# Kernel tuning notes

Measured on AMD Instinct MI355X. Metric: run time of the kernel, lower is better.

The kernel has to match this reference:

```python
import jax, jax.numpy as jnp
import numpy as np

D_MODEL = 2048
N_HEADS = 16
HEAD_DIM = D_MODEL // N_HEADS
B, T = 2, 2048


def setup_inputs() -> dict:
    key = jax.random.key(0)
    ks = jax.random.split(key, 7)
    s = 0.02
    return {
        "x": jax.random.normal(ks[0], (B, T, D_MODEL), dtype=jnp.float32),
        "w_qkv": jax.random.normal(ks[1], (D_MODEL, 3 * D_MODEL), dtype=jnp.float32) * s,
        "w_proj": jax.random.normal(ks[2], (D_MODEL, D_MODEL), dtype=jnp.float32) * s,
        "w_ff1": jax.random.normal(ks[3], (D_MODEL, 4 * D_MODEL), dtype=jnp.float32) * s,
        "b_ff1": jnp.zeros((4 * D_MODEL,), dtype=jnp.float32),
        "w_ff2": jax.random.normal(ks[4], (4 * D_MODEL, D_MODEL), dtype=jnp.float32) * s,
        "b_ff2": jnp.zeros((D_MODEL,), dtype=jnp.float32),
    }


def reference(x, w_qkv, w_proj, w_ff1, b_ff1, w_ff2, b_ff2):
    Bs, Ts, C = x.shape
    H, hd = N_HEADS, HEAD_DIM
    # fused qkv projection
    qkv = jnp.einsum("btc,cd->btd", x, w_qkv)
    q, k, v = jnp.split(qkv, 3, axis=-1)
    # (B, T, C) -> (B, H, T, hd)
    q = q.reshape(Bs, Ts, H, hd).transpose(0, 2, 1, 3)
    k = k.reshape(Bs, Ts, H, hd).transpose(0, 2, 1, 3)
    v = v.reshape(Bs, Ts, H, hd).transpose(0, 2, 1, 3)
    # paged KV write + gather round-trip (empty cache, n_kv_head == n_heads)
    # is the identity on k, v; attention is causal SDPA over the full cache.
    scale = 1.0 / jnp.sqrt(jnp.asarray(hd, dtype=x.dtype))
    scores = jnp.einsum("bhqd,bhkd->bhqk", q, k) * scale
    causal = jnp.tril(jnp.ones((Ts, Ts), dtype=bool))
    scores = jnp.where(causal, scores, jnp.finfo(scores.dtype).min)
    attn = jax.nn.softmax(scores, axis=-1)
    out = jnp.einsum("bhqk,bhkd->bhqd", attn, v)  # (B, H, T, hd)
    out = out.transpose(0, 2, 1, 3).reshape(Bs, Ts, C)
    attn_out = jnp.einsum("btc,cd->btd", out, w_proj)
    # feed-forward with exact GELU (torch nn.GELU default)
    h = jax.nn.gelu(jnp.einsum("btc,cf->btf", x, w_ff1) + b_ff1, approximate=False)
    ff_out = jnp.einsum("btf,fc->btc", h, w_ff2) + b_ff2
    return x + attn_out + ff_out
```

## Files before the change

kernel.cpp:

```cpp
#include <hip/hip_runtime.h>
#include <hip/hip_bf16.h>
#include <cmath>

typedef __bf16 bf16x8 __attribute__((ext_vector_type(8)));
typedef float f32x4 __attribute__((ext_vector_type(4)));
typedef unsigned short u16;
typedef unsigned int u32;

#define DEV __device__ __forceinline__

static constexpr int BB = 2;
static constexpr int T = 2048;
static constexpr int DM = 2048;
static constexpr int NH = 16;
static constexpr int HD = 128;
static constexpr int FF = 8192;
static constexpr int M = BB * T;
static constexpr int NQKV = 3 * DM;

DEV u16 f2b(float f) {
  u32 u = __builtin_bit_cast(u32, f);
  u = (u + 0x7FFFu + ((u >> 16) & 1u)) >> 16;
  return (u16)u;
}
DEV float b2f(u16 h) {
  u32 u = ((u32)h) << 16;
  return __builtin_bit_cast(float, u);
}

DEV void gload16(const u16* g, const u16* l) {
  __builtin_amdgcn_global_load_lds(
      (const __attribute__((address_space(1))) void*)(uintptr_t)g,
      (__attribute__((address_space(3))) void*)(unsigned)(uintptr_t)l,
      16, 0, 0);
}


__global__ void cvt_f32_to_bf16(const float* __restrict__ in, u16* __restrict__ out, int n4) {
  int i = blockIdx.x * blockDim.x + threadIdx.x;
  if (i >= n4) return;
  float4 v = reinterpret_cast<const float4*>(in)[i];
  ushort4 o;
  o.x = f2b(v.x); o.y = f2b(v.y); o.z = f2b(v.z); o.w = f2b(v.w);
  reinterpret_cast<ushort4*>(out)[i] = o;
}

__global__ void transpose_cvt(const float* __restrict__ W, u16* __restrict__ Wt, int K, int N) {
  __shared__ float tile[32][33];
  int nb = blockIdx.x * 32, kb = blockIdx.y * 32;
  int tx = threadIdx.x & 31, ty = threadIdx.x >> 5;
#pragma unroll
  for (int r = 0; r < 32; r += 8)
    tile[ty + r][tx] = W[(size_t)(kb + ty + r) * N + nb + tx];
  __syncthreads();
#pragma unroll
  for (int r = 0; r < 32; r += 8)
    Wt[(size_t)(nb + ty + r) * K + kb + tx] = f2b(tile[tx][ty + r]);
}

template <int EPI>
__global__ __launch_bounds__(512, 2) void gemm8(
    const u16* __restrict__ A, const u16* __restrict__ Bt, int Ndim, int K, int gx,
    u16* __restrict__ out_bf, const float* __restrict__ bias) {
  __shared__ __align__(16) u16 lds[2 * 32768];
  const int t = threadIdx.x;
  const int nwg = gridDim.x, cpx = nwg >> 3;
  const int wg = (blockIdx.x & 7) * cpx + (blockIdx.x >> 3);
  const int m0 = (wg / gx) * 256, n0 = (wg % gx) * 256;
  const int wave = t >> 6, lane = t & 63;
  const int wm = wave >> 2, wn = wave & 3;
  const int lr = lane & 15, lk = lane >> 4;

  const int srow = t >> 3;
  const int sc8 = ((t & 7) ^ (srow & 7)) * 8;
  const u16* gA = &A[(size_t)(m0 + srow) * K + sc8];
  const u16* gB = &Bt[(size_t)(n0 + srow) * K + sc8];
  const int wls = wave * 512;

  u16* buf0 = lds;
  u16* buf1 = lds + 32768;

#define STAGE_A(buf, h, kt)                                                      \
  {                                                                              \
    gload16(gA + (size_t)((h) * 128) * K + (kt) * 64, (buf) + (h) * 8192 + wls); \
    gload16(gA + (size_t)((h) * 128 + 64) * K + (kt) * 64,                       \
            (buf) + (h) * 8192 + 4096 + wls);                                    \
  }
#define STAGE_B(buf, h, kt)                                                      \
  {                                                                              \
    gload16(gB + (size_t)((h) * 128) * K + (kt) * 64,                            \
            (buf) + 16384 + (h) * 8192 + wls);                                   \
    gload16(gB + (size_t)((h) * 128 + 64) * K + (kt) * 64,                       \
            (buf) + 16384 + (h) * 8192 + 4096 + wls);                            \
  }
#define PH_PRE                          \
  __builtin_amdgcn_sched_barrier(0);    \
  __builtin_amdgcn_s_barrier();         \
  __builtin_amdgcn_sched_barrier(0);    \
  __builtin_amdgcn_s_setprio(1);
#define PH_POST                         \
  __builtin_amdgcn_s_setprio(0);        \
  __builtin_amdgcn_sched_barrier(0);    \
  __builtin_amdgcn_s_barrier();         \
  __builtin_amdgcn_sched_barrier(0);

  const int NT = K >> 6;

  STAGE_A(buf0, 0, 0); STAGE_A(buf0, 1, 0);
  STAGE_B(buf0, 0, 0); STAGE_B(buf0, 1, 0);
  STAGE_A(buf1, 0, 1); STAGE_B(buf1, 0, 1);
  __builtin_amdgcn_sched_barrier(0);
  asm volatile("s_waitcnt vmcnt(4)" ::: "memory");
  __builtin_amdgcn_s_barrier();
  __builtin_amdgcn_sched_barrier(0);

  f32x4 acc[8][4] = {};
  const int aBase = (wm * 128 + lr) * 64;
  const int bBase = 16384 + (wn * 64 + lr) * 64;
  const int c0 = (lk ^ (lr & 7)) * 8;
  const int c1 = ((4 + lk) ^ (lr & 7)) * 8;

  u16* cur = buf0;
  u16* alt = buf1;
  bf16x8 af[4][2], bq0[2][2], bq1[2][2];

  for (int kt = 0; kt < NT; ++kt) {
#pragma unroll
    for (int i = 0; i < 4; ++i) {
      af[i][0] = *(const bf16x8*)&cur[aBase + i * 1024 + c0];
      af[i][1] = *(const bf16x8*)&cur[aBase + i * 1024 + c1];
    }
#pragma unroll
    for (int j = 0; j < 2; ++j) {
      bq0[j][0] = *(const bf16x8*)&cur[bBase + j * 1024 + c0];
      bq0[j][1] = *(const bf16x8*)&cur[bBase + j * 1024 + c1];
    }
    if (kt + 1 < NT) STAGE_A(alt, 1, kt + 1);
    PH_PRE;
#pragma unroll
    for (int i = 0; i < 4; ++i)
#pragma unroll
      for (int j = 0; j < 2; ++j)
#pragma unroll
        for (int kk = 0; kk < 2; ++kk)
          acc[i][j] = __builtin_amdgcn_mfma_f32_16x16x32_bf16(af[i][kk], bq0[j][kk], acc[i][j], 0, 0, 0);
    PH_POST;
#pragma unroll
    for (int j = 0; j < 2; ++j) {
      bq1[j][0] = *(const bf16x8*)&cur[bBase + (2 + j) * 1024 + c0];
      bq1[j][1] = *(const bf16x8*)&cur[bBase + (2 + j) * 1024 + c1];
    }
    if (kt + 1 < NT) STAGE_B(alt, 1, kt + 1);
    PH_PRE;
#pragma unroll
    for (int i = 0; i < 4; ++i)
#pragma unroll
      for (int j = 0; j < 2; ++j)
#pragma unroll
        for (int kk = 0; kk < 2; ++kk)
          acc[i][2 + j] = __builtin_amdgcn_mfma_f32_16x16x32_bf16(af[i][kk], bq1[j][kk], acc[i][2 + j], 0, 0, 0);
    PH_POST;
#pragma unroll
    for (int i = 0; i < 4; ++i) {
      af[i][0] = *(const bf16x8*)&cur[aBase + (4 + i) * 1024 + c0];
      af[i][1] = *(const bf16x8*)&cur[aBase + (4 + i) * 1024 + c1];
    }
    if (kt + 2 < NT) STAGE_A(cur, 0, kt + 2);
    PH_PRE;
#pragma unroll
    for (int i = 0; i < 4; ++i)
#pragma unroll
      for (int j = 0; j < 2; ++j)
#pragma unroll
        for (int kk = 0; kk < 2; ++kk)
          acc[4 + i][2 + j] = __builtin_amdgcn_mfma_f32_16x16x32_bf16(af[i][kk], bq1[j][kk], acc[4 + i][2 + j], 0, 0, 0);
    PH_POST;
    if (kt + 2 < NT) STAGE_B(cur, 0, kt + 2);
    PH_PRE;
#pragma unroll
    for (int i = 0; i < 4; ++i)
#pragma unroll
      for (int j = 0; j < 2; ++j)
#pragma unroll
        for (int kk = 0; kk < 2; ++kk)
          acc[4 + i][j] = __builtin_amdgcn_mfma_f32_16x16x32_bf16(af[i][kk], bq0[j][kk], acc[4 + i][j], 0, 0, 0);
    __builtin_amdgcn_s_setprio(0);
    __builtin_amdgcn_sched_barrier(0);
    if (kt + 2 < NT)      asm volatile("s_waitcnt vmcnt(4)" ::: "memory");
    else if (kt + 1 < NT) asm volatile("s_waitcnt vmcnt(0)" ::: "memory");
    __builtin_amdgcn_s_barrier();
    __builtin_amdgcn_sched_barrier(0);
    u16* tmp = cur; cur = alt; alt = tmp;
  }
#undef STAGE_A
#undef STAGE_B
#undef PH_PRE
#undef PH_POST

#pragma unroll
  for (int i = 0; i < 8; ++i) {
#pragma unroll
    for (int j = 0; j < 4; ++j) {
#pragma unroll
      for (int r = 0; r < 4; ++r) {
        int gr = m0 + wm * 128 + i * 16 + (lane >> 4) * 4 + r;
        int gc = n0 + wn * 64 + j * 16 + (lane & 15);
        float v = acc[i][j][r];
        if constexpr (EPI == 0) {
          int part = gc >> 11, cc = gc & 2047;
          int head = cc >> 7, d = cc & 127;
          int b = gr >> 11, tt = gr & 2047;
          out_bf[(size_t)part * M * DM + (((size_t)(b * NH + head) * T + tt) * HD + d)] = f2b(v);
        } else {
          v += bias[gc];
          float u = v * (v * v * 0.044715f + 1.0f) * 0.7978845608028654f;
          float e = exp2f(u * 2.885390081777927f);
          float th = 1.0f - 2.0f / (e + 1.0f);
          v = 0.5f * v * (1.0f + th);
          out_bf[(size_t)gr * Ndim + gc] = f2b(v);
        }
      }
    }
  }
}

template <int EPI>
__global__ __launch_bounds__(512, 4) void gemm_bf16(
    const u16* __restrict__ A, const u16* __restrict__ Bt, int Ndim, int K, int gx,
    u16* __restrict__ out_bf, float* __restrict__ out_f32,
    const float* __restrict__ bias,
    const float* __restrict__ resid_f32, const u16* __restrict__ resid_bf) {
  __shared__ __align__(16) u16 lds[3 * (256 + 128) * 32];
  const int t = threadIdx.x;
  const int nwg = gridDim.x, cpx = nwg >> 3;
  const int wg = (blockIdx.x & 7) * cpx + (blockIdx.x >> 3);
  const int m0 = (wg / gx) * 256, n0 = (wg % gx) * 128;
  const int wave = t >> 6, lane = t & 63;
  const int wm = wave >> 1, wn = wave & 1;
  const int lr = lane & 15, lk = lane >> 4;

  u16* cA = lds;                   u16* cB = lds + 8192;
  u16* nA = lds + 12288;           u16* nB = lds + 12288 + 8192;
  u16* sA = lds + 2 * 12288;       u16* sB = lds + 2 * 12288 + 8192;

  const int sk = ((lane & 3) ^ ((lane >> 3) & 3)) * 8;
  const u16* gA0 = &A[(size_t)(m0 + wave * 16 + (lane >> 2)) * K + sk];
  const u16* gA1 = gA0 + (size_t)128 * K;
  const u16* gB0 = &Bt[(size_t)(n0 + wave * 16 + (lane >> 2)) * K + sk];

  const int wbase = wave * 512;

  auto stage = [&](u16* dA, u16* dB) {
    gload16(gA0, dA + wbase);
    gload16(gA1, dA + 4096 + wbase);
    gload16(gB0, dB + wbase);
    gA0 += 32; gA1 += 32; gB0 += 32;
  };

  const int NT = K >> 5;

  stage(cA, cB);
  stage(nA, nB);
  __builtin_amdgcn_sched_barrier(0);
  asm volatile("s_waitcnt vmcnt(3)" ::: "memory");
  __builtin_amdgcn_s_barrier();
  __builtin_amdgcn_sched_barrier(0);

  f32x4 acc[4][4] = {};
  const int rcol = (lk ^ ((lr >> 1) & 3)) * 8;

  for (int kt = 0; kt < NT; ++kt) {
    if (kt + 2 < NT) stage(sA, sB);
    bf16x8 af[4], bfr[4];
#pragma unroll
    for (int i = 0; i < 4; ++i) {
      af[i]  = *reinterpret_cast<const bf16x8*>(&cA[(wm * 64 + i * 16 + lr) * 32 + rcol]);
      bfr[i] = *reinterpret_cast<const bf16x8*>(&cB[(wn * 64 + i * 16 + lr) * 32 + rcol]);
    }
#pragma unroll
    for (int i = 0; i < 4; ++i)
#pragma unroll
      for (int j = 0; j < 4; ++j)
        acc[i][j] = __builtin_amdgcn_mfma_f32_16x16x32_bf16(af[i], bfr[j], acc[i][j], 0, 0, 0);
    if (kt + 1 < NT) {
      __builtin_amdgcn_sched_barrier(0);
      if (kt + 2 < NT) asm volatile("s_waitcnt vmcnt(3)" ::: "memory");
      else             asm volatile("s_waitcnt vmcnt(0)" ::: "memory");
      __builtin_amdgcn_s_barrier();
      __builtin_amdgcn_sched_barrier(0);
      u16* tA = cA; u16* tB = cB;
      cA = nA; cB = nB; nA = sA; nB = sB; sA = tA; sB = tB;
    }
  }

#pragma unroll
  for (int i = 0; i < 4; ++i) {
#pragma unroll
    for (int j = 0; j < 4; ++j) {
#pragma unroll
      for (int r = 0; r < 4; ++r) {
        int gr = m0 + wm * 64 + i * 16 + (lane >> 4) * 4 + r;
        int gc = n0 + wn * 64 + j * 16 + (lane & 15);
        float v = acc[i][j][r];
        if constexpr (EPI == 1) {
          out_bf[(size_t)gr * Ndim + gc] = f2b(v);
        } else if constexpr (EPI == 3) {
          v += bias[gc] + resid_f32[(size_t)gr * Ndim + gc] + b2f(resid_bf[(size_t)gr * Ndim + gc]);
          out_f32[(size_t)gr * Ndim + gc] = v;
        } else {
          int hh = gr >> 7, d = gr & 127;
          int b = gc >> 11, tt = gc & 2047;
          out_bf[((size_t)(b * NH + hh) * HD + d) * T + tt] = f2b(v);
        }
      }
    }
  }
}

__global__ __launch_bounds__(256) void attn_fwd(
    const u16* __restrict__ qg, const u16* __restrict__ kg,
    const u16* __restrict__ vt, u16* __restrict__ outg) {
  __shared__ __align__(16) u16 lK[64 * 128];
  __shared__ __align__(16) u16 lVt[128 * 64];
  __shared__ __align__(16) u16 lP[4][16 * 72];
  const int t = threadIdx.x;
  const int qi = gridDim.x - 1 - blockIdx.x;
  const int bh = blockIdx.y;
  const int wv = t >> 6, lane = t & 63;
  const int lc = lane & 15, lg = lane >> 4;
  const size_t base = (size_t)bh * T * HD;
  const size_t vbase = (size_t)bh * HD * T;
  const int q0 = qi * 64;

  bf16x8 qf[4];
#pragma unroll
  for (int kk = 0; kk < 4; ++kk)
    qf[kk] = *reinterpret_cast<const bf16x8*>(
        &qg[base + (size_t)(q0 + wv * 16 + lc) * HD + kk * 32 + lg * 8]);

  f32x4 oacc[8] = {};
  float mrow[4], lrow[4];
#pragma unroll
  for (int r = 0; r < 4; ++r) { mrow[r] = -INFINITY; lrow[r] = 0.f; }

  const float scaleL = 0.08838834764831845f * 1.4426950408889634f;
  const int ntiles = qi + 1;
  for (int kt = 0; kt < ntiles; ++kt) {
    __syncthreads();
#pragma unroll
    for (int h = 0; h < 4; ++h) {
      int row = h * 16 + wv * 4 + (lane >> 4);
      int sb = ((lane & 15) * 16) ^ ((row & 7) << 4);
      gload16(&kg[base + (size_t)(kt * 64 + row) * HD + (sb >> 1)],
              (const u16*)((const char*)lK + (h * 256 + wv * 64) * 16));
    }
#pragma unroll
    for (int h = 0; h < 4; ++h) {
      int row = h * 32 + wv * 8 + (lane >> 3);
      int sb = ((lane & 7) * 16) ^ ((row & 7) << 4);
      gload16(&vt[vbase + (size_t)row * T + kt * 64 + (sb >> 1)],
              (const u16*)((const char*)lVt + (h * 256 + wv * 64) * 16));
    }
    __syncthreads();

    f32x4 s[4] = {};
#pragma unroll
    for (int nf = 0; nf < 4; ++nf) {
      int krow = nf * 16 + lc;
#pragma unroll
      for (int kk = 0; kk < 4; ++kk) {
        int dbyte = kk * 64 + lg * 16;
        bf16x8 kf = *reinterpret_cast<const bf16x8*>(
            reinterpret_cast<const char*>(lK) + krow * 256 + (dbyte ^ ((krow & 7) << 4)));
        s[nf] = __builtin_amdgcn_mfma_f32_16x16x32_bf16(qf[kk], kf, s[nf], 0, 0, 0);
      }
    }

    float rmax[4];
#pragma unroll
    for (int r = 0; r < 4; ++r) rmax[r] = -INFINITY;
#pragma unroll
    for (int nf = 0; nf < 4; ++nf) {
      int col = kt * 64 + nf * 16 + lc;
#pragma unroll
      for (int r = 0; r < 4; ++r) {
        int row = q0 + wv * 16 + lg * 4 + r;
        float sv = s[nf][r] * scaleL;
        if (col > row) sv = -INFINITY;
        s[nf][r] = sv;
        rmax[r] = fmaxf(rmax[r], sv);
      }
    }
#pragma unroll
    for (int mk = 1; mk < 16; mk <<= 1)
#pragma unroll
      for (int r = 0; r < 4; ++r)
        rmax[r] = fmaxf(rmax[r], __shfl_xor(rmax[r], mk));

    int need = 0;
#pragma unroll
    for (int r = 0; r < 4; ++r) need |= (rmax[r] > mrow[r] + 11.5f) ? 1 : 0;
    if (__any(need)) {
      float corr[4];
#pragma unroll
      for (int r = 0; r < 4; ++r) {
        float mnew = fmaxf(mrow[r], rmax[r]);
        corr[r] = exp2f(mrow[r] - mnew);
        mrow[r] = mnew;
        lrow[r] *= corr[r];
      }
#pragma unroll
      for (int dc = 0; dc < 8; ++dc)
#pragma unroll
        for (int r = 0; r < 4; ++r) oacc[dc][r] *= corr[r];
    }

#pragma unroll
    for (int nf = 0; nf < 4; ++nf) {
#pragma unroll
      for (int r = 0; r < 4; ++r) {
        float p = exp2f(s[nf][r] - mrow[r]);
        lrow[r] += p;
        lP[wv][(lg * 4 + r) * 72 + nf * 16 + lc] = f2b(p);
      }
    }
    bf16x8 pa[2];
#pragma unroll
    for (int kk = 0; kk < 2; ++kk)
      pa[kk] = *reinterpret_cast<const bf16x8*>(&lP[wv][lc * 72 + kk * 32 + lg * 8]);
#pragma unroll
    for (int dc = 0; dc < 8; ++dc) {
#pragma unroll
      for (int kk = 0; kk < 2; ++kk) {
        int vrow = dc * 16 + lc;
        int off = (kk * 64 + lg * 16) ^ ((vrow & 7) << 4);
        bf16x8 vf = *reinterpret_cast<const bf16x8*>(
            reinterpret_cast<const char*>(lVt) + vrow * 128 + off);
        oacc[dc] = __builtin_amdgcn_mfma_f32_16x16x32_bf16(pa[kk], vf, oacc[dc], 0, 0, 0);
      }
    }
  }

#pragma unroll
  for (int mk = 1; mk < 16; mk <<= 1)
#pragma unroll
    for (int r = 0; r < 4; ++r) lrow[r] += __shfl_xor(lrow[r], mk);

  const int b = bh >> 4, hh = bh & 15;
#pragma unroll
  for (int dc = 0; dc < 8; ++dc)
#pragma unroll
    for (int r = 0; r < 4; ++r) {
      int tt = q0 + wv * 16 + lg * 4 + r;
      int d = dc * 16 + lc;
      float o = oacc[dc][r] / lrow[r];
      outg[(size_t)(b * T + tt) * DM + hh * HD + d] = f2b(o);
    }
}


extern "C" void kernel_launch(void* const* d_in, const int* in_sizes, int n_in,
                              void* d_out, int out_size, void* d_ws, size_t ws_size,
                              hipStream_t stream) {
  const float* x      = (const float*)d_in[0];
  const float* w_qkv  = (const float*)d_in[1];
  const float* w_proj = (const float*)d_in[2];
  const float* w_ff1  = (const float*)d_in[3];
  const float* b_ff1  = (const float*)d_in[4];
  const float* w_ff2  = (const float*)d_in[5];
  const float* b_ff2  = (const float*)d_in[6];
  float* out = (float*)d_out;

  u16* ws = (u16*)d_ws;
  size_t o = 0;
  u16* x_bf      = ws + o; o += (size_t)M * DM;
  u16* wqkv_t    = ws + o; o += (size_t)NQKV * DM;
  u16* wproj_t   = ws + o; o += (size_t)DM * DM;
  u16* wff1_t    = ws + o; o += (size_t)FF * DM;
  u16* wff2_t    = ws + o; o += (size_t)DM * FF;
  u16* attn_proj = ws + o; o += (size_t)M * DM;
  u16* qbuf      = ws + o;
  u16* kbuf      = qbuf + (size_t)M * DM;
  u16* vtbuf     = kbuf + (size_t)M * DM;
  u16* attn_out  = vtbuf + (size_t)M * DM;
  u16* hbuf      = qbuf;

  cvt_f32_to_bf16<<<(M * DM / 4 + 255) / 256, 256, 0, stream>>>(x, x_bf, M * DM / 4);
  transpose_cvt<<<dim3(NQKV / 32, DM / 32), 256, 0, stream>>>(w_qkv, wqkv_t, DM, NQKV);
  transpose_cvt<<<dim3(DM / 32, DM / 32), 256, 0, stream>>>(w_proj, wproj_t, DM, DM);
  transpose_cvt<<<dim3(FF / 32, DM / 32), 256, 0, stream>>>(w_ff1, wff1_t, DM, FF);
  transpose_cvt<<<dim3(DM / 32, FF / 32), 256, 0, stream>>>(w_ff2, wff2_t, FF, DM);

  gemm8<0><<<256, 512, 0, stream>>>(x_bf, wqkv_t, 4096, DM, 16, qbuf, nullptr);

  gemm_bf16<4><<<256, 512, 0, stream>>>(
      wqkv_t + (size_t)4096 * DM, x_bf, M, DM, 32, vtbuf, nullptr, nullptr, nullptr, nullptr);

  attn_fwd<<<dim3(T / 64, BB * NH), 256, 0, stream>>>(qbuf, kbuf, vtbuf, attn_out);

  gemm_bf16<1><<<256, 512, 0, stream>>>(
      attn_out, wproj_t, DM, DM, 16, attn_proj, nullptr, nullptr, nullptr, nullptr);

  gemm8<2><<<512, 512, 0, stream>>>(x_bf, wff1_t, FF, DM, 32, hbuf, b_ff1);

  gemm_bf16<3><<<256, 512, 0, stream>>>(
      hbuf, wff2_t, DM, FF, 16, nullptr, out, b_ff2, x, attn_proj);
}
```

Baseline: 655.8 us.

## Widen attention query tile to 128 rows with 8 waves; vectorize weight transpose

The attention kernel now uses 512 threads (8 waves) per block, covering 128 query rows, so each K/V tile loaded into LDS is shared by twice as many query rows and total K/V traffic per head is halved. The MFMA sections are wrapped in s_setprio to favour matrix issue over the other waves. The weight transpose-and-convert kernel now does float4 loads and ushort4 stores. The trade-off is coarser causal granularity, since each block also processes the partially masked diagonal tiles, and fewer blocks in the grid.

After: 668.2 us. Within noise of the previous version (+1.9%).

```diff
diff --git a/kernel.cpp b/kernel.cpp
--- a/kernel.cpp
+++ b/kernel.cpp
@@ -48,14 +48,15 @@
 __global__ void transpose_cvt(const float* __restrict__ W, u16* __restrict__ Wt, int K, int N) {
   __shared__ float tile[32][33];
   int nb = blockIdx.x * 32, kb = blockIdx.y * 32;
-  int tx = threadIdx.x & 31, ty = threadIdx.x >> 5;
-#pragma unroll
-  for (int r = 0; r < 32; r += 8)
-    tile[ty + r][tx] = W[(size_t)(kb + ty + r) * N + nb + tx];
+  int r = threadIdx.x >> 3;
+  int c4 = (threadIdx.x & 7) * 4;
+  float4 v = *reinterpret_cast<const float4*>(&W[(size_t)(kb + r) * N + nb + c4]);
+  tile[r][c4] = v.x; tile[r][c4 + 1] = v.y; tile[r][c4 + 2] = v.z; tile[r][c4 + 3] = v.w;
   __syncthreads();
-#pragma unroll
-  for (int r = 0; r < 32; r += 8)
-    Wt[(size_t)(nb + ty + r) * K + kb + tx] = f2b(tile[tx][ty + r]);
+  ushort4 o;
+  o.x = f2b(tile[c4][r]);     o.y = f2b(tile[c4 + 1][r]);
+  o.z = f2b(tile[c4 + 2][r]); o.w = f2b(tile[c4 + 3][r]);
+  *reinterpret_cast<ushort4*>(&Wt[(size_t)(nb + r) * K + kb + c4]) = o;
 }
 
 template <int EPI>
@@ -317,12 +318,12 @@
   }
 }
 
-__global__ __launch_bounds__(256) void attn_fwd(
+__global__ __launch_bounds__(512) void attn_fwd(
     const u16* __restrict__ qg, const u16* __restrict__ kg,
     const u16* __restrict__ vt, u16* __restrict__ outg) {
   __shared__ __align__(16) u16 lK[64 * 128];
   __shared__ __align__(16) u16 lVt[128 * 64];
-  __shared__ __align__(16) u16 lP[4][16 * 72];
+  __shared__ __align__(16) u16 lP[8][16 * 72];
   const int t = threadIdx.x;
   const int qi = gridDim.x - 1 - blockIdx.x;
   const int bh = blockIdx.y;
@@ -330,7 +331,7 @@
   const int lc = lane & 15, lg = lane >> 4;
   const size_t base = (size_t)bh * T * HD;
   const size_t vbase = (size_t)bh * HD * T;
-  const int q0 = qi * 64;
+  const int q0 = qi * 128;
 
   bf16x8 qf[4];
 #pragma unroll
@@ -344,26 +345,29 @@
   for (int r = 0; r < 4; ++r) { mrow[r] = -INFINITY; lrow[r] = 0.f; }
 
   const float scaleL = 0.08838834764831845f * 1.4426950408889634f;
-  const int ntiles = qi + 1;
+  const int ntiles = 2 * qi + 2;
   for (int kt = 0; kt < ntiles; ++kt) {
     __syncthreads();
 #pragma unroll
-    for (int h = 0; h < 4; ++h) {
-      int row = h * 16 + wv * 4 + (lane >> 4);
-      int sb = ((lane & 15) * 16) ^ ((row & 7) << 4);
+    for (int h = 0; h < 2; ++h) {
+      int c = t + h * 512;
+      int row = c >> 4;
+      int sb = ((c & 15) * 16) ^ ((row & 7) << 4);
       gload16(&kg[base + (size_t)(kt * 64 + row) * HD + (sb >> 1)],
-              (const u16*)((const char*)lK + (h * 256 + wv * 64) * 16));
-    }
-#pragma unroll
-    for (int h = 0; h < 4; ++h) {
-      int row = h * 32 + wv * 8 + (lane >> 3);
-      int sb = ((lane & 7) * 16) ^ ((row & 7) << 4);
+              (const u16*)((const char*)lK + ((h * 8 + wv) * 64) * 16));
+    }
+#pragma unroll
+    for (int h = 0; h < 2; ++h) {
+      int c = t + h * 512;
+      int row = c >> 3;
+      int sb = ((c & 7) * 16) ^ ((row & 7) << 4);
       gload16(&vt[vbase + (size_t)row * T + kt * 64 + (sb >> 1)],
-              (const u16*)((const char*)lVt + (h * 256 + wv * 64) * 16));
+              (const u16*)((const char*)lVt + ((h * 8 + wv) * 64) * 16));
     }
     __syncthreads();
 
     f32x4 s[4] = {};
+    __builtin_amdgcn_s_setprio(1);
 #pragma unroll
     for (int nf = 0; nf < 4; ++nf) {
       int krow = nf * 16 + lc;
@@ -375,6 +379,7 @@
         s[nf] = __builtin_amdgcn_mfma_f32_16x16x32_bf16(qf[kk], kf, s[nf], 0, 0, 0);
       }
     }
+    __builtin_amdgcn_s_setprio(0);
 
     float rmax[4];
 #pragma unroll
@@ -428,6 +433,7 @@
 #pragma unroll
     for (int kk = 0; kk < 2; ++kk)
       pa[kk] = *reinterpret_cast<const bf16x8*>(&lP[wv][lc * 72 + kk * 32 + lg * 8]);
+    __builtin_amdgcn_s_setprio(1);
 #pragma unroll
     for (int dc = 0; dc < 8; ++dc) {
 #pragma unroll
@@ -439,6 +445,7 @@
         oacc[dc] = __builtin_amdgcn_mfma_f32_16x16x32_bf16(pa[kk], vf, oacc[dc], 0, 0, 0);
       }
     }
+    __builtin_amdgcn_s_setprio(0);
   }
 
 #pragma unroll
@@ -496,7 +503,7 @@
   gemm_bf16<4><<<256, 512, 0, stream>>>(
       wqkv_t + (size_t)4096 * DM, x_bf, M, DM, 32, vtbuf, nullptr, nullptr, nullptr, nullptr);
 
-  attn_fwd<<<dim3(T / 64, BB * NH), 256, 0, stream>>>(qbuf, kbuf, vtbuf, attn_out);
+  attn_fwd<<<dim3(T / 128, BB * NH), 512, 0, stream>>>(qbuf, kbuf, vtbuf, attn_out);
 
   gemm_bf16<1><<<256, 512, 0, stream>>>(
       attn_out, wproj_t, DM, DM, 16, attn_proj, nullptr, nullptr, nullptr, nullptr);
```
